# Performance work log

Hardware: AMD Instinct MI355X
Metric: run time of the kernel (lower is better)

Reference implementation:

```python
import jax, jax.numpy as jnp
import numpy as np

H_GRID, W_GRID = 32, 32
KH, KW = 7, 11
NUM_HEADS = 8


def local_window_mask(H, W, kh, kw):
    # Token (h,w) may attend to (h',w') iff |h-h'|<=kh//2 and |w-w'|<=kw//2
    # (equivalent to the padded/cropped construction in the torch module).
    hh = jnp.arange(H)
    ww = jnp.arange(W)
    ok_h = jnp.abs(hh[:, None] - hh[None, :]) <= kh // 2  # [H,H]
    ok_w = jnp.abs(ww[:, None] - ww[None, :]) <= kw // 2  # [W,W]
    ok = ok_h[:, None, :, None] & ok_w[None, :, None, :]  # [H,W,H,W]
    ok = ok.reshape(H * W, H * W)
    return jnp.where(ok, 0.0, -jnp.inf)[None, None]  # [1,1,N,N]


def setup_inputs() -> dict:
    key = jax.random.key(0)
    k1, k2, k3, k4, k5 = jax.random.split(key, 5)
    B, N, E = 8, H_GRID * W_GRID, 256
    return {
        "x": jax.random.normal(k1, (B, N, E), dtype=jnp.float32),
        "qkv_w": jax.random.normal(k2, (3 * E, E), dtype=jnp.float32) * 0.02,
        "qkv_b": jax.random.normal(k3, (3 * E,), dtype=jnp.float32) * 0.02,
        "proj_w": jax.random.normal(k4, (E, E), dtype=jnp.float32) * 0.02,
        "proj_b": jax.random.normal(k5, (E,), dtype=jnp.float32) * 0.02,
    }


def reference(x, qkv_w, qkv_b, proj_w, proj_b):
    B, N, E = x.shape
    dh = E // NUM_HEADS
    scale = E ** (-0.5)  # note: embed_dim scaling, as in the original module
    qkv = x @ qkv_w.T + qkv_b                       # [B,N,3E]
    qkv = qkv.reshape(B, N, 3, NUM_HEADS, dh).transpose(2, 0, 3, 1, 4)
    q, k, v = qkv[0] * scale, qkv[1], qkv[2]        # [B,H,N,dh]
    attn = jnp.einsum('bhnd,bhmd->bhnm', q, k)      # [B,H,N,N]
    attn = attn + local_window_mask(H_GRID, W_GRID, KH, KW)
    attn = jax.nn.softmax(attn, axis=-1)
    out = jnp.einsum('bhnm,bhmd->bhnd', attn, v)    # [B,H,N,dh]
    out = out.transpose(0, 2, 1, 3).reshape(B, N, E)
    return out @ proj_w.T + proj_b
```

## Files before the change

### kernel.cpp

```cpp
#include <hip/hip_runtime.h>
#include <math.h>

constexpr int Bb = 8;
constexpr int Ns = 1024;
constexpr int Es = 256;
constexpr int NH = 8;
constexpr int DH = 32;
constexpr int Mrows = Bb * Ns;
constexpr int NX = Mrows * Es;
constexpr int NQ = 3 * Es * Es;
constexpr int NP = Es * Es;

typedef __bf16 bf16x8 __attribute__((ext_vector_type(8)));
typedef float  f32x4  __attribute__((ext_vector_type(4)));
union U4B8 { uint4 u; bf16x8 b; unsigned short s[8]; };

__device__ __forceinline__ unsigned short f2bf(float f) {
    union { float f; unsigned u; } c; c.f = f;
    unsigned r = (c.u + 0x7FFFu + ((c.u >> 16) & 1u)) >> 16;
    return (unsigned short)r;
}
__device__ __forceinline__ float bf2f(unsigned short h) {
    union { unsigned u; float f; } c; c.u = ((unsigned)h) << 16;
    return c.f;
}

#define GLD 72
#define PST 232


__global__ __launch_bounds__(256, 8)
void cast_all(const float* __restrict__ x, const float* __restrict__ wq,
              const float* __restrict__ wp, unsigned short* __restrict__ xb,
              unsigned short* __restrict__ wqb, unsigned short* __restrict__ wpb)
{
    int i = (blockIdx.x * 256 + threadIdx.x) * 8;
    const float* src; unsigned short* dst;
    if (i < NX)            { src = x  + i;             dst = xb  + i; }
    else if (i < NX + NQ)  { src = wq + (i - NX);      dst = wqb + (i - NX); }
    else                   { src = wp + (i - NX - NQ); dst = wpb + (i - NX - NQ); }
    float4 f0 = *(const float4*)src;
    float4 f1 = *(const float4*)(src + 4);
    U4B8 u;
    u.s[0] = f2bf(f0.x); u.s[1] = f2bf(f0.y); u.s[2] = f2bf(f0.z); u.s[3] = f2bf(f0.w);
    u.s[4] = f2bf(f1.x); u.s[5] = f2bf(f1.y); u.s[6] = f2bf(f1.z); u.s[7] = f2bf(f1.w);
    *(uint4*)dst = u.u;
}

__global__ __launch_bounds__(256, 8)
void qkv_gemm(const unsigned short* __restrict__ A, const unsigned short* __restrict__ W,
              const float* __restrict__ qkv_b,
              unsigned short* __restrict__ qo, unsigned short* __restrict__ ko,
              unsigned short* __restrict__ vto)
{
    __shared__ unsigned short As[64 * GLD];
    __shared__ unsigned short Ws[64 * GLD];

    const int t = threadIdx.x;
    const int m0 = (blockIdx.x & 127) * 64;
    const int j0 = (blockIdx.x >> 7) * 64;

    const int srow = t >> 2;
    const int scol = (t & 3) * 16;

    const int lane = t & 63;
    const int wave = t >> 6;
    const int wm = (wave & 1) * 32;
    const int wn = (wave >> 1) * 32;
    const int fm = lane & 15;
    const int fq = lane >> 4;

    f32x4 acc[2][2];
    #pragma unroll
    for (int i = 0; i < 2; i++)
        #pragma unroll
        for (int j = 0; j < 2; j++)
            acc[i][j] = (f32x4){0.f, 0.f, 0.f, 0.f};

    const unsigned short* Arow = A + (size_t)(m0 + srow) * Es;
    const unsigned short* Wrow = W + (size_t)(j0 + srow) * Es;

    for (int k0 = 0; k0 < Es; k0 += 64) {
        uint4 a0 = *(const uint4*)(Arow + k0 + scol);
        uint4 a1 = *(const uint4*)(Arow + k0 + scol + 8);
        uint4 w0 = *(const uint4*)(Wrow + k0 + scol);
        uint4 w1 = *(const uint4*)(Wrow + k0 + scol + 8);
        __syncthreads();
        *(uint4*)&As[srow * GLD + scol]     = a0;
        *(uint4*)&As[srow * GLD + scol + 8] = a1;
        *(uint4*)&Ws[srow * GLD + scol]     = w0;
        *(uint4*)&Ws[srow * GLD + scol + 8] = w1;
        __syncthreads();
        #pragma unroll
        for (int ks = 0; ks < 64; ks += 32) {
            U4B8 af0, af1, bf0, bf1;
            af0.u = *(const uint4*)&As[(wm +      fm) * GLD + ks + fq * 8];
            af1.u = *(const uint4*)&As[(wm + 16 + fm) * GLD + ks + fq * 8];
            bf0.u = *(const uint4*)&Ws[(wn +      fm) * GLD + ks + fq * 8];
            bf1.u = *(const uint4*)&Ws[(wn + 16 + fm) * GLD + ks + fq * 8];
            acc[0][0] = __builtin_amdgcn_mfma_f32_16x16x32_bf16(af0.b, bf0.b, acc[0][0], 0, 0, 0);
            acc[0][1] = __builtin_amdgcn_mfma_f32_16x16x32_bf16(af0.b, bf1.b, acc[0][1], 0, 0, 0);
            acc[1][0] = __builtin_amdgcn_mfma_f32_16x16x32_bf16(af1.b, bf0.b, acc[1][0], 0, 0, 0);
            acc[1][1] = __builtin_amdgcn_mfma_f32_16x16x32_bf16(af1.b, bf1.b, acc[1][1], 0, 0, 0);
        }
    }

    #pragma unroll
    for (int mt = 0; mt < 2; mt++) {
        #pragma unroll
        for (int nt = 0; nt < 2; nt++) {
            #pragma unroll
            for (int r = 0; r < 4; r++) {
                int row = m0 + wm + mt * 16 + fq * 4 + r;
                int col = j0 + wn + nt * 16 + fm;
                float val = acc[mt][nt][r] + qkv_b[col];
                int part = col >> 8;
                int head = (col >> 5) & 7;
                int d = col & 31;
                int b = row >> 10;
                int n = row & 1023;
                int bh = b * NH + head;
                if (part == 0)
                    qo[((size_t)bh * Ns + n) * DH + d] = f2bf(val * 0.0625f);
                else if (part == 1)
                    ko[((size_t)bh * Ns + n) * DH + d] = f2bf(val);
                else
                    vto[((size_t)bh * DH + d) * Ns + n] = f2bf(val);
            }
        }
    }
}

__global__ __launch_bounds__(256, 6)
void attn_mfma2(const unsigned short* __restrict__ qb, const unsigned short* __restrict__ kb,
                const unsigned short* __restrict__ vtb, unsigned short* __restrict__ aob)
{
    __shared__ unsigned short Pb[32 * PST];
    __shared__ float psum[2][32];

    const int blk = blockIdx.x;
    const int b   = blk & 7;
    const int u   = blk >> 3;
    const int h   = u & 7;
    const int hq  = u >> 3;
    const int bh  = b * NH + h;

    const int t   = threadIdx.x;
    const int lane = t & 63;
    const int w    = t >> 6;
    const int fm = lane & 15;
    const int fq = lane >> 4;

    int n0c = (hq - 3) * 32;
    n0c = n0c < 0 ? 0 : (n0c > Ns - 224 ? Ns - 224 : n0c);

    const int qbase = (w & 1) * 16;
    const int sel   = w >> 1;
    const int dbase = (w >> 1) * 16;

    const unsigned short* vrow = vtb + ((size_t)bh * DH + dbase + fm) * Ns;
    uint4 vpre[7];
    #pragma unroll
    for (int i = 0; i < 7; i++)
        vpre[i] = *(const uint4*)(vrow + n0c + i * 32 + fq * 8);

    U4B8 qa;
    qa.u = *(const uint4*)(qb + ((size_t)bh * Ns + hq * 32 + qbase + fm) * DH + fq * 8);

    f32x4 sv[7];
    #pragma unroll
    for (int i = 0; i < 7; i++) {
        int kt = sel + 2 * i;
        U4B8 kf;
        kf.u = *(const uint4*)(kb + ((size_t)bh * Ns + n0c + kt * 16 + fm) * DH + fq * 8);
        sv[i] = __builtin_amdgcn_mfma_f32_16x16x32_bf16(qa.b, kf.b, (f32x4){0.f,0.f,0.f,0.f}, 0, 0, 0);
    }

    float sm[4] = {0.f, 0.f, 0.f, 0.f};
    #pragma unroll
    for (int i = 0; i < 7; i++) {
        int kt = sel + 2 * i;
        int g = n0c + kt * 16 + fm;
        int gh = g >> 5, gw = g & 31;
        int dhh = gh - hq;
        bool okh = (dhh >= -3) && (dhh <= 3);
        #pragma unroll
        for (int r = 0; r < 4; r++) {
            int qc = qbase + fq * 4 + r;
            int dww = gw - qc;
            bool ok = okh && (dww >= -5) && (dww <= 5);
            float p = ok ? __expf(sv[i][r]) : 0.f;
            unsigned short pu = f2bf(p);
            Pb[qc * PST + kt * 16 + fm] = pu;
            sm[r] += bf2f(pu);
        }
    }
    #pragma unroll
    for (int r = 0; r < 4; r++)
        #pragma unroll
        for (int m = 1; m < 16; m <<= 1)
            sm[r] += __shfl_xor(sm[r], m);
    if (fm == 0) {
        #pragma unroll
        for (int r = 0; r < 4; r++)
            psum[sel][qbase + fq * 4 + r] = sm[r];
    }
    __syncthreads();

    f32x4 acc = (f32x4){0.f, 0.f, 0.f, 0.f};
    #pragma unroll
    for (int i = 0; i < 7; i++) {
        U4B8 pa, vb;
        pa.u = *(const uint4*)&Pb[(qbase + fm) * PST + i * 32 + fq * 8];
        vb.u = vpre[i];
        acc = __builtin_amdgcn_mfma_f32_16x16x32_bf16(pa.b, vb.b, acc, 0, 0, 0);
    }

    #pragma unroll
    for (int r = 0; r < 4; r++) {
        int qq = qbase + fq * 4 + r;
        float inv = 1.f / (psum[0][qq] + psum[1][qq]);
        aob[((size_t)(b * Ns) + hq * 32 + qq) * Es + h * DH + dbase + fm] = f2bf(acc[r] * inv);
    }
}

__global__ __launch_bounds__(256, 8)
void proj_gemm(const unsigned short* __restrict__ A, const unsigned short* __restrict__ Wb,
               const float* __restrict__ bias, float* __restrict__ out)
{
    __shared__ unsigned short As[64 * GLD];
    __shared__ unsigned short Ws[64 * GLD];

    const int t = threadIdx.x;
    const int m0 = (blockIdx.x & 127) * 64;
    const int j0 = (blockIdx.x >> 7) * 64;

    const int srow = t >> 2;
    const int scol = (t & 3) * 16;

    const int lane = t & 63;
    const int wave = t >> 6;
    const int wm = (wave & 1) * 32;
    const int wn = (wave >> 1) * 32;
    const int fm = lane & 15;
    const int fq = lane >> 4;

    f32x4 acc[2][2];
    #pragma unroll
    for (int i = 0; i < 2; i++)
        #pragma unroll
        for (int j = 0; j < 2; j++)
            acc[i][j] = (f32x4){0.f, 0.f, 0.f, 0.f};

    const unsigned short* Arow = A + (size_t)(m0 + srow) * Es;
    const unsigned short* Wrow = Wb + (size_t)(j0 + srow) * Es;

    for (int k0 = 0; k0 < Es; k0 += 64) {
        uint4 a0 = *(const uint4*)(Arow + k0 + scol);
        uint4 a1 = *(const uint4*)(Arow + k0 + scol + 8);
        uint4 w0 = *(const uint4*)(Wrow + k0 + scol);
        uint4 w1 = *(const uint4*)(Wrow + k0 + scol + 8);
        __syncthreads();
        *(uint4*)&As[srow * GLD + scol]     = a0;
        *(uint4*)&As[srow * GLD + scol + 8] = a1;
        *(uint4*)&Ws[srow * GLD + scol]     = w0;
        *(uint4*)&Ws[srow * GLD + scol + 8] = w1;
        __syncthreads();
        #pragma unroll
        for (int ks = 0; ks < 64; ks += 32) {
            U4B8 af0, af1, bf0, bf1;
            af0.u = *(const uint4*)&As[(wm +      fm) * GLD + ks + fq * 8];
            af1.u = *(const uint4*)&As[(wm + 16 + fm) * GLD + ks + fq * 8];
            bf0.u = *(const uint4*)&Ws[(wn +      fm) * GLD + ks + fq * 8];
            bf1.u = *(const uint4*)&Ws[(wn + 16 + fm) * GLD + ks + fq * 8];
            acc[0][0] = __builtin_amdgcn_mfma_f32_16x16x32_bf16(af0.b, bf0.b, acc[0][0], 0, 0, 0);
            acc[0][1] = __builtin_amdgcn_mfma_f32_16x16x32_bf16(af0.b, bf1.b, acc[0][1], 0, 0, 0);
            acc[1][0] = __builtin_amdgcn_mfma_f32_16x16x32_bf16(af1.b, bf0.b, acc[1][0], 0, 0, 0);
            acc[1][1] = __builtin_amdgcn_mfma_f32_16x16x32_bf16(af1.b, bf1.b, acc[1][1], 0, 0, 0);
        }
    }

    #pragma unroll
    for (int mt = 0; mt < 2; mt++) {
        #pragma unroll
        for (int nt = 0; nt < 2; nt++) {
            #pragma unroll
            for (int r = 0; r < 4; r++) {
                int row = m0 + wm + mt * 16 + fq * 4 + r;
                int col = j0 + wn + nt * 16 + fm;
                out[(size_t)row * Es + col] = acc[mt][nt][r] + bias[col];
            }
        }
    }
}

extern "C" void kernel_launch(void* const* d_in, const int* in_sizes, int n_in,
                              void* d_out, int out_size, void* d_ws, size_t ws_size,
                              hipStream_t stream) {
    const float* x      = (const float*)d_in[0];
    const float* qkv_w  = (const float*)d_in[1];
    const float* qkv_b  = (const float*)d_in[2];
    const float* proj_w = (const float*)d_in[3];
    const float* proj_b = (const float*)d_in[4];
    float* out = (float*)d_out;

    unsigned short* xb  = (unsigned short*)d_ws;
    unsigned short* wqb = xb + NX;
    unsigned short* pwb = wqb + NQ;
    unsigned short* qb  = pwb + NP;
    unsigned short* kb  = qb + NX;
    unsigned short* vtb = kb + NX;
    unsigned short* aob = vtb + NX;

    cast_all<<<dim3((NX + NQ + NP) / 8 / 256), dim3(256), 0, stream>>>(
        x, qkv_w, proj_w, xb, wqb, pwb);

    qkv_gemm<<<dim3(1536), dim3(256), 0, stream>>>(xb, wqb, qkv_b, qb, kb, vtb);

    attn_mfma2<<<dim3(Bb * NH * 32), dim3(256), 0, stream>>>(qb, kb, vtb, aob);

    proj_gemm<<<dim3(128 * 4), dim3(256), 0, stream>>>(aob, pwb, proj_b, out);
}
```

Baseline: 100.4 us.

## Load GEMM MFMA fragments directly from global memory, dropping LDS staging

Both the QKV and projection GEMMs no longer stage A and W tiles through shared memory with barriers. Each wave now loads its MFMA operand fragments straight from global memory in a fully unrolled K loop. The launch-bounds occupancy hint drops from 8 to 4 to leave room for the extra registers. This removes LDS round-trips and __syncthreads, but reuse across waves now relies on L1/L2 caches and the global loads are 16-byte strided per row.

```diff
diff --git a/kernel.cpp b/kernel.cpp
--- a/kernel.cpp
+++ b/kernel.cpp
@@ -25,7 +25,6 @@
     return c.f;
 }
 
-#define GLD 72
 #define PST 232
 
 
@@ -47,21 +46,15 @@
     *(uint4*)dst = u.u;
 }
 
-__global__ __launch_bounds__(256, 8)
+__global__ __launch_bounds__(256, 4)
 void qkv_gemm(const unsigned short* __restrict__ A, const unsigned short* __restrict__ W,
               const float* __restrict__ qkv_b,
               unsigned short* __restrict__ qo, unsigned short* __restrict__ ko,
               unsigned short* __restrict__ vto)
 {
-    __shared__ unsigned short As[64 * GLD];
-    __shared__ unsigned short Ws[64 * GLD];
-
     const int t = threadIdx.x;
     const int m0 = (blockIdx.x & 127) * 64;
     const int j0 = (blockIdx.x >> 7) * 64;
-
-    const int srow = t >> 2;
-    const int scol = (t & 3) * 16;
 
     const int lane = t & 63;
     const int wave = t >> 6;
@@ -70,6 +63,11 @@
     const int fm = lane & 15;
     const int fq = lane >> 4;
 
+    const unsigned short* Ar0 = A + (size_t)(m0 + wm + fm) * Es + fq * 8;
+    const unsigned short* Ar1 = Ar0 + 16 * Es;
+    const unsigned short* Wr0 = W + (size_t)(j0 + wn + fm) * Es + fq * 8;
+    const unsigned short* Wr1 = Wr0 + 16 * Es;
+
     f32x4 acc[2][2];
     #pragma unroll
     for (int i = 0; i < 2; i++)
@@ -77,32 +75,17 @@
         for (int j = 0; j < 2; j++)
             acc[i][j] = (f32x4){0.f, 0.f, 0.f, 0.f};
 
-    const unsigned short* Arow = A + (size_t)(m0 + srow) * Es;
-    const unsigned short* Wrow = W + (size_t)(j0 + srow) * Es;
-
-    for (int k0 = 0; k0 < Es; k0 += 64) {
-        uint4 a0 = *(const uint4*)(Arow + k0 + scol);
-        uint4 a1 = *(const uint4*)(Arow + k0 + scol + 8);
-        uint4 w0 = *(const uint4*)(Wrow + k0 + scol);
-        uint4 w1 = *(const uint4*)(Wrow + k0 + scol + 8);
-        __syncthreads();
-        *(uint4*)&As[srow * GLD + scol]     = a0;
-        *(uint4*)&As[srow * GLD + scol + 8] = a1;
-        *(uint4*)&Ws[srow * GLD + scol]     = w0;
-        *(uint4*)&Ws[srow * GLD + scol + 8] = w1;
-        __syncthreads();
-        #pragma unroll
-        for (int ks = 0; ks < 64; ks += 32) {
-            U4B8 af0, af1, bf0, bf1;
-            af0.u = *(const uint4*)&As[(wm +      fm) * GLD + ks + fq * 8];
-            af1.u = *(const uint4*)&As[(wm + 16 + fm) * GLD + ks + fq * 8];
-            bf0.u = *(const uint4*)&Ws[(wn +      fm) * GLD + ks + fq * 8];
-            bf1.u = *(const uint4*)&Ws[(wn + 16 + fm) * GLD + ks + fq * 8];
-            acc[0][0] = __builtin_amdgcn_mfma_f32_16x16x32_bf16(af0.b, bf0.b, acc[0][0], 0, 0, 0);
-            acc[0][1] = __builtin_amdgcn_mfma_f32_16x16x32_bf16(af0.b, bf1.b, acc[0][1], 0, 0, 0);
-            acc[1][0] = __builtin_amdgcn_mfma_f32_16x16x32_bf16(af1.b, bf0.b, acc[1][0], 0, 0, 0);
-            acc[1][1] = __builtin_amdgcn_mfma_f32_16x16x32_bf16(af1.b, bf1.b, acc[1][1], 0, 0, 0);
-        }
+    #pragma unroll
+    for (int ks = 0; ks < Es; ks += 32) {
+        U4B8 af0, af1, bf0, bf1;
+        af0.u = *(const uint4*)(Ar0 + ks);
+        af1.u = *(const uint4*)(Ar1 + ks);
+        bf0.u = *(const uint4*)(Wr0 + ks);
+        bf1.u = *(const uint4*)(Wr1 + ks);
+        acc[0][0] = __builtin_amdgcn_mfma_f32_16x16x32_bf16(af0.b, bf0.b, acc[0][0], 0, 0, 0);
+        acc[0][1] = __builtin_amdgcn_mfma_f32_16x16x32_bf16(af0.b, bf1.b, acc[0][1], 0, 0, 0);
+        acc[1][0] = __builtin_amdgcn_mfma_f32_16x16x32_bf16(af1.b, bf0.b, acc[1][0], 0, 0, 0);
+        acc[1][1] = __builtin_amdgcn_mfma_f32_16x16x32_bf16(af1.b, bf1.b, acc[1][1], 0, 0, 0);
     }
 
     #pragma unroll
@@ -224,19 +207,13 @@
     }
 }
 
-__global__ __launch_bounds__(256, 8)
+__global__ __launch_bounds__(256, 4)
 void proj_gemm(const unsigned short* __restrict__ A, const unsigned short* __restrict__ Wb,
                const float* __restrict__ bias, float* __restrict__ out)
 {
-    __shared__ unsigned short As[64 * GLD];
-    __shared__ unsigned short Ws[64 * GLD];
-
     const int t = threadIdx.x;
     const int m0 = (blockIdx.x & 127) * 64;
     const int j0 = (blockIdx.x >> 7) * 64;
-
-    const int srow = t >> 2;
-    const int scol = (t & 3) * 16;
 
     const int lane = t & 63;
     const int wave = t >> 6;
@@ -245,6 +222,11 @@
     const int fm = lane & 15;
     const int fq = lane >> 4;
 
+    const unsigned short* Ar0 = A  + (size_t)(m0 + wm + fm) * Es + fq * 8;
+    const unsigned short* Ar1 = Ar0 + 16 * Es;
+    const unsigned short* Wr0 = Wb + (size_t)(j0 + wn + fm) * Es + fq * 8;
+    const unsigned short* Wr1 = Wr0 + 16 * Es;
+
     f32x4 acc[2][2];
     #pragma unroll
     for (int i = 0; i < 2; i++)
@@ -252,32 +234,17 @@
         for (int j = 0; j < 2; j++)
             acc[i][j] = (f32x4){0.f, 0.f, 0.f, 0.f};
 
-    const unsigned short* Arow = A + (size_t)(m0 + srow) * Es;
-    const unsigned short* Wrow = Wb + (size_t)(j0 + srow) * Es;
-
-    for (int k0 = 0; k0 < Es; k0 += 64) {
-        uint4 a0 = *(const uint4*)(Arow + k0 + scol);
-        uint4 a1 = *(const uint4*)(Arow + k0 + scol + 8);
-        uint4 w0 = *(const uint4*)(Wrow + k0 + scol);
-        uint4 w1 = *(const uint4*)(Wrow + k0 + scol + 8);
-        __syncthreads();
-        *(uint4*)&As[srow * GLD + scol]     = a0;
-        *(uint4*)&As[srow * GLD + scol + 8] = a1;
-        *(uint4*)&Ws[srow * GLD + scol]     = w0;
-        *(uint4*)&Ws[srow * GLD + scol + 8] = w1;
-        __syncthreads();
-        #pragma unroll
-        for (int ks = 0; ks < 64; ks += 32) {
-            U4B8 af0, af1, bf0, bf1;
-            af0.u = *(const uint4*)&As[(wm +      fm) * GLD + ks + fq * 8];
-            af1.u = *(const uint4*)&As[(wm + 16 + fm) * GLD + ks + fq * 8];
-            bf0.u = *(const uint4*)&Ws[(wn +      fm) * GLD + ks + fq * 8];
-            bf1.u = *(const uint4*)&Ws[(wn + 16 + fm) * GLD + ks + fq * 8];
-            acc[0][0] = __builtin_amdgcn_mfma_f32_16x16x32_bf16(af0.b, bf0.b, acc[0][0], 0, 0, 0);
-            acc[0][1] = __builtin_amdgcn_mfma_f32_16x16x32_bf16(af0.b, bf1.b, acc[0][1], 0, 0, 0);
-            acc[1][0] = __builtin_amdgcn_mfma_f32_16x16x32_bf16(af1.b, bf0.b, acc[1][0], 0, 0, 0);
-            acc[1][1] = __builtin_amdgcn_mfma_f32_16x16x32_bf16(af1.b, bf1.b, acc[1][1], 0, 0, 0);
-        }
+    #pragma unroll
+    for (int ks = 0; ks < Es; ks += 32) {
+        U4B8 af0, af1, bf0, bf1;
+        af0.u = *(const uint4*)(Ar0 + ks);
+        af1.u = *(const uint4*)(Ar1 + ks);
+        bf0.u = *(const uint4*)(Wr0 + ks);
+        bf1.u = *(const uint4*)(Wr1 + ks);
+        acc[0][0] = __builtin_amdgcn_mfma_f32_16x16x32_bf16(af0.b, bf0.b, acc[0][0], 0, 0, 0);
+        acc[0][1] = __builtin_amdgcn_mfma_f32_16x16x32_bf16(af0.b, bf1.b, acc[0][1], 0, 0, 0);
+        acc[1][0] = __builtin_amdgcn_mfma_f32_16x16x32_bf16(af1.b, bf0.b, acc[1][0], 0, 0, 0);
+        acc[1][1] = __builtin_amdgcn_mfma_f32_16x16x32_bf16(af1.b, bf1.b, acc[1][1], 0, 0, 0);
     }
 
     #pragma unroll
```

New measurement: 121.4 us. +20.9%, slower.

## Fuse local-window attention with output projection into one kernel

Applied to the files above, without the earlier changes.

Merges the attention kernel and the projection GEMM into a single kernel. Each 512-thread block handles one batch and one 32-query row strip across all 8 heads, stages the attention output in shared memory, then multiplies it by the projection weights read directly from global memory. This drops the global round-trip of the attention output and one kernel launch. The cost is a grid of only 256 blocks with more work per block and lower occupancy, which may leave part of the GPU idle.

```diff
diff --git a/kernel.cpp b/kernel.cpp
--- a/kernel.cpp
+++ b/kernel.cpp
@@ -26,7 +26,8 @@
 }
 
 #define GLD 72
-#define PST 232
+#define PSTW 228
+#define AOST 264
 
 
 __global__ __launch_bounds__(256, 8)
@@ -131,153 +132,144 @@
     }
 }
 
-__global__ __launch_bounds__(256, 6)
-void attn_mfma2(const unsigned short* __restrict__ qb, const unsigned short* __restrict__ kb,
-                const unsigned short* __restrict__ vtb, unsigned short* __restrict__ aob)
+__global__ __launch_bounds__(512, 2)
+void attn_proj(const unsigned short* __restrict__ qb, const unsigned short* __restrict__ kb,
+               const unsigned short* __restrict__ vtb, const unsigned short* __restrict__ pw,
+               const float* __restrict__ proj_b, float* __restrict__ out)
 {
-    __shared__ unsigned short Pb[32 * PST];
-    __shared__ float psum[2][32];
+    __shared__ __align__(16) unsigned short SM[8 * 16 * PSTW];
+
+    const int t    = threadIdx.x;
+    const int w    = t >> 6;
+    const int lane = t & 63;
+    const int fm   = lane & 15;
+    const int fq   = lane >> 4;
 
     const int blk = blockIdx.x;
     const int b   = blk & 7;
-    const int u   = blk >> 3;
-    const int h   = u & 7;
-    const int hq  = u >> 3;
-    const int bh  = b * NH + h;
-
-    const int t   = threadIdx.x;
-    const int lane = t & 63;
-    const int w    = t >> 6;
-    const int fm = lane & 15;
-    const int fq = lane >> 4;
+    const int hq  = blk >> 3;
 
     int n0c = (hq - 3) * 32;
     n0c = n0c < 0 ? 0 : (n0c > Ns - 224 ? Ns - 224 : n0c);
 
     const int qbase = (w & 1) * 16;
-    const int sel   = w >> 1;
-    const int dbase = (w >> 1) * 16;
-
-    const unsigned short* vrow = vtb + ((size_t)bh * DH + dbase + fm) * Ns;
-    uint4 vpre[7];
-    #pragma unroll
-    for (int i = 0; i < 7; i++)
-        vpre[i] = *(const uint4*)(vrow + n0c + i * 32 + fq * 8);
-
-    U4B8 qa;
-    qa.u = *(const uint4*)(qb + ((size_t)bh * Ns + hq * 32 + qbase + fm) * DH + fq * 8);
-
-    f32x4 sv[7];
-    #pragma unroll
-    for (int i = 0; i < 7; i++) {
-        int kt = sel + 2 * i;
-        U4B8 kf;
-        kf.u = *(const uint4*)(kb + ((size_t)bh * Ns + n0c + kt * 16 + fm) * DH + fq * 8);
-        sv[i] = __builtin_amdgcn_mfma_f32_16x16x32_bf16(qa.b, kf.b, (f32x4){0.f,0.f,0.f,0.f}, 0, 0, 0);
-    }
-
-    float sm[4] = {0.f, 0.f, 0.f, 0.f};
-    #pragma unroll
-    for (int i = 0; i < 7; i++) {
-        int kt = sel + 2 * i;
-        int g = n0c + kt * 16 + fm;
-        int gh = g >> 5, gw = g & 31;
-        int dhh = gh - hq;
-        bool okh = (dhh >= -3) && (dhh <= 3);
-        #pragma unroll
-        for (int r = 0; r < 4; r++) {
-            int qc = qbase + fq * 4 + r;
-            int dww = gw - qc;
-            bool ok = okh && (dww >= -5) && (dww <= 5);
-            float p = ok ? __expf(sv[i][r]) : 0.f;
-            unsigned short pu = f2bf(p);
-            Pb[qc * PST + kt * 16 + fm] = pu;
-            sm[r] += bf2f(pu);
-        }
-    }
-    #pragma unroll
-    for (int r = 0; r < 4; r++)
-        #pragma unroll
-        for (int m = 1; m < 16; m <<= 1)
-            sm[r] += __shfl_xor(sm[r], m);
-    if (fm == 0) {
+    unsigned short* Pw = SM + w * 16 * PSTW;
+
+    unsigned opack[2][2][2];
+
+    #pragma unroll
+    for (int r2 = 0; r2 < 2; r2++) {
+        const int h  = (w >> 1) + 4 * r2;
+        const int bh = b * NH + h;
+
+        U4B8 vpre[2][7];
+        #pragma unroll
+        for (int d2 = 0; d2 < 2; d2++) {
+            const unsigned short* vrow = vtb + ((size_t)bh * DH + d2 * 16 + fm) * Ns;
+            #pragma unroll
+            for (int i = 0; i < 7; i++)
+                vpre[d2][i].u = *(const uint4*)(vrow + n0c + i * 32 + fq * 8);
+        }
+
+        U4B8 qa;
+        qa.u = *(const uint4*)(qb + ((size_t)bh * Ns + hq * 32 + qbase + fm) * DH + fq * 8);
+
+        f32x4 sv[14];
+        #pragma unroll
+        for (int kt = 0; kt < 14; kt++) {
+            U4B8 kf;
+            kf.u = *(const uint4*)(kb + ((size_t)bh * Ns + n0c + kt * 16 + fm) * DH + fq * 8);
+            sv[kt] = __builtin_amdgcn_mfma_f32_16x16x32_bf16(qa.b, kf.b, (f32x4){0.f,0.f,0.f,0.f}, 0, 0, 0);
+        }
+
+        __syncthreads();
+
+        float sm4[4] = {0.f, 0.f, 0.f, 0.f};
+        #pragma unroll
+        for (int kt = 0; kt < 14; kt++) {
+            int g = n0c + kt * 16 + fm;
+            int gh = g >> 5, gw = g & 31;
+            int dhh = gh - hq;
+            bool okh = (dhh >= -3) && (dhh <= 3);
+            #pragma unroll
+            for (int r = 0; r < 4; r++) {
+                int qc = qbase + fq * 4 + r;
+                int dww = gw - qc;
+                bool ok = okh && (dww >= -5) && (dww <= 5);
+                float p = ok ? __expf(sv[kt][r]) : 0.f;
+                unsigned short pu = f2bf(p);
+                Pw[(fq * 4 + r) * PSTW + kt * 16 + fm] = pu;
+                sm4[r] += bf2f(pu);
+            }
+        }
         #pragma unroll
         for (int r = 0; r < 4; r++)
-            psum[sel][qbase + fq * 4 + r] = sm[r];
-    }
+            #pragma unroll
+            for (int m = 1; m < 16; m <<= 1)
+                sm4[r] += __shfl_xor(sm4[r], m);
+        float inv[4];
+        #pragma unroll
+        for (int r = 0; r < 4; r++)
+            inv[r] = 1.f / sm4[r];
+
+        __syncthreads();
+
+        #pragma unroll
+        for (int d2 = 0; d2 < 2; d2++) {
+            f32x4 acc = (f32x4){0.f, 0.f, 0.f, 0.f};
+            #pragma unroll
+            for (int i = 0; i < 7; i++) {
+                U4B8 pa;
+                pa.u = *(const uint4*)&Pw[fm * PSTW + i * 32 + fq * 8];
+                acc = __builtin_amdgcn_mfma_f32_16x16x32_bf16(pa.b, vpre[d2][i].b, acc, 0, 0, 0);
+            }
+            unsigned p0 = (unsigned)f2bf(acc[0] * inv[0]) | ((unsigned)f2bf(acc[1] * inv[1]) << 16);
+            unsigned p1 = (unsigned)f2bf(acc[2] * inv[2]) | ((unsigned)f2bf(acc[3] * inv[3]) << 16);
+            opack[r2][d2][0] = p0;
+            opack[r2][d2][1] = p1;
+        }
+    }
+
     __syncthreads();
 
-    f32x4 acc = (f32x4){0.f, 0.f, 0.f, 0.f};
-    #pragma unroll
-    for (int i = 0; i < 7; i++) {
-        U4B8 pa, vb;
-        pa.u = *(const uint4*)&Pb[(qbase + fm) * PST + i * 32 + fq * 8];
-        vb.u = vpre[i];
-        acc = __builtin_amdgcn_mfma_f32_16x16x32_bf16(pa.b, vb.b, acc, 0, 0, 0);
-    }
-
-    #pragma unroll
-    for (int r = 0; r < 4; r++) {
-        int qq = qbase + fq * 4 + r;
-        float inv = 1.f / (psum[0][qq] + psum[1][qq]);
-        aob[((size_t)(b * Ns) + hq * 32 + qq) * Es + h * DH + dbase + fm] = f2bf(acc[r] * inv);
-    }
-}
-
-__global__ __launch_bounds__(256, 8)
-void proj_gemm(const unsigned short* __restrict__ A, const unsigned short* __restrict__ Wb,
-               const float* __restrict__ bias, float* __restrict__ out)
-{
-    __shared__ unsigned short As[64 * GLD];
-    __shared__ unsigned short Ws[64 * GLD];
-
-    const int t = threadIdx.x;
-    const int m0 = (blockIdx.x & 127) * 64;
-    const int j0 = (blockIdx.x >> 7) * 64;
-
-    const int srow = t >> 2;
-    const int scol = (t & 3) * 16;
-
-    const int lane = t & 63;
-    const int wave = t >> 6;
-    const int wm = (wave & 1) * 32;
-    const int wn = (wave >> 1) * 32;
-    const int fm = lane & 15;
-    const int fq = lane >> 4;
-
-    f32x4 acc[2][2];
+    unsigned short* ao = SM;
+    #pragma unroll
+    for (int r2 = 0; r2 < 2; r2++) {
+        int h = (w >> 1) + 4 * r2;
+        #pragma unroll
+        for (int d2 = 0; d2 < 2; d2++) {
+            #pragma unroll
+            for (int r = 0; r < 4; r++) {
+                unsigned word = opack[r2][d2][r >> 1];
+                unsigned short v = (unsigned short)((r & 1) ? (word >> 16) : (word & 0xFFFFu));
+                ao[(qbase + fq * 4 + r) * AOST + h * 32 + d2 * 16 + fm] = v;
+            }
+        }
+    }
+
+    __syncthreads();
+
+    const unsigned short* Wr0 = pw + (size_t)(w * 32 + fm) * Es + fq * 8;
+    const unsigned short* Wr1 = Wr0 + 16 * Es;
+
+    f32x4 pacc[2][2];
     #pragma unroll
     for (int i = 0; i < 2; i++)
         #pragma unroll
         for (int j = 0; j < 2; j++)
-            acc[i][j] = (f32x4){0.f, 0.f, 0.f, 0.f};
-
-    const unsigned short* Arow = A + (size_t)(m0 + srow) * Es;
-    const unsigned short* Wrow = Wb + (size_t)(j0 + srow) * Es;
-
-    for (int k0 = 0; k0 < Es; k0 += 64) {
-        uint4 a0 = *(const uint4*)(Arow + k0 + scol);
-        uint4 a1 = *(const uint4*)(Arow + k0 + scol + 8);
-        uint4 w0 = *(const uint4*)(Wrow + k0 + scol);
-        uint4 w1 = *(const uint4*)(Wrow + k0 + scol + 8);
-        __syncthreads();
-        *(uint4*)&As[srow * GLD + scol]     = a0;
-        *(uint4*)&As[srow * GLD + scol + 8] = a1;
-        *(uint4*)&Ws[srow * GLD + scol]     = w0;
-        *(uint4*)&Ws[srow * GLD + scol + 8] = w1;
-        __syncthreads();
-        #pragma unroll
-        for (int ks = 0; ks < 64; ks += 32) {
-            U4B8 af0, af1, bf0, bf1;
-            af0.u = *(const uint4*)&As[(wm +      fm) * GLD + ks + fq * 8];
-            af1.u = *(const uint4*)&As[(wm + 16 + fm) * GLD + ks + fq * 8];
-            bf0.u = *(const uint4*)&Ws[(wn +      fm) * GLD + ks + fq * 8];
-            bf1.u = *(const uint4*)&Ws[(wn + 16 + fm) * GLD + ks + fq * 8];
-            acc[0][0] = __builtin_amdgcn_mfma_f32_16x16x32_bf16(af0.b, bf0.b, acc[0][0], 0, 0, 0);
-            acc[0][1] = __builtin_amdgcn_mfma_f32_16x16x32_bf16(af0.b, bf1.b, acc[0][1], 0, 0, 0);
-            acc[1][0] = __builtin_amdgcn_mfma_f32_16x16x32_bf16(af1.b, bf0.b, acc[1][0], 0, 0, 0);
-            acc[1][1] = __builtin_amdgcn_mfma_f32_16x16x32_bf16(af1.b, bf1.b, acc[1][1], 0, 0, 0);
-        }
+            pacc[i][j] = (f32x4){0.f, 0.f, 0.f, 0.f};
+
+    #pragma unroll
+    for (int ks = 0; ks < Es; ks += 32) {
+        U4B8 a0, a1, w0, w1;
+        a0.u = *(const uint4*)&ao[(fm)      * AOST + ks + fq * 8];
+        a1.u = *(const uint4*)&ao[(16 + fm) * AOST + ks + fq * 8];
+        w0.u = *(const uint4*)(Wr0 + ks);
+        w1.u = *(const uint4*)(Wr1 + ks);
+        pacc[0][0] = __builtin_amdgcn_mfma_f32_16x16x32_bf16(a0.b, w0.b, pacc[0][0], 0, 0, 0);
+        pacc[0][1] = __builtin_amdgcn_mfma_f32_16x16x32_bf16(a0.b, w1.b, pacc[0][1], 0, 0, 0);
+        pacc[1][0] = __builtin_amdgcn_mfma_f32_16x16x32_bf16(a1.b, w0.b, pacc[1][0], 0, 0, 0);
+        pacc[1][1] = __builtin_amdgcn_mfma_f32_16x16x32_bf16(a1.b, w1.b, pacc[1][1], 0, 0, 0);
     }
 
     #pragma unroll
@@ -286,9 +278,9 @@
         for (int nt = 0; nt < 2; nt++) {
             #pragma unroll
             for (int r = 0; r < 4; r++) {
-                int row = m0 + wm + mt * 16 + fq * 4 + r;
-                int col = j0 + wn + nt * 16 + fm;
-                out[(size_t)row * Es + col] = acc[mt][nt][r] + bias[col];
+                int row = hq * 32 + mt * 16 + fq * 4 + r;
+                int col = w * 32 + nt * 16 + fm;
+                out[((size_t)b * Ns + row) * Es + col] = pacc[mt][nt][r] + proj_b[col];
             }
         }
     }
@@ -310,14 +302,11 @@
     unsigned short* qb  = pwb + NP;
     unsigned short* kb  = qb + NX;
     unsigned short* vtb = kb + NX;
-    unsigned short* aob = vtb + NX;
 
     cast_all<<<dim3((NX + NQ + NP) / 8 / 256), dim3(256), 0, stream>>>(
         x, qkv_w, proj_w, xb, wqb, pwb);
 
     qkv_gemm<<<dim3(1536), dim3(256), 0, stream>>>(xb, wqb, qkv_b, qb, kb, vtb);
 
-    attn_mfma2<<<dim3(Bb * NH * 32), dim3(256), 0, stream>>>(qb, kb, vtb, aob);
-
-    proj_gemm<<<dim3(128 * 4), dim3(256), 0, stream>>>(aob, pwb, proj_b, out);
-}
+    attn_proj<<<dim3(256), dim3(512), 0, stream>>>(qb, kb, vtb, pwb, proj_b, out);
+}
```

Measured after the change: 103.7 us. 1.03x slower.
